# Performance work log

Hardware: AMD Instinct MI355X
Metric: run time of the kernel (lower is better)

The kernel has to match this reference:

```python
import jax, jax.numpy as jnp
import numpy as np

B, S, E, H = 2, 2048, 1024, 16
D = E // H  # head_dim = 64
SCALE = D ** -0.5
NEG = -1e9


def setup_inputs() -> dict:
    key = jax.random.key(0)
    ks = jax.random.split(key, 10)
    hidden_states = jax.random.normal(ks[0], (B, S, E), dtype=jnp.float32)
    # CLIP-style additive causal mask [B, 1, L, S]
    causal = jnp.where(jnp.tril(jnp.ones((S, S), dtype=bool)), 0.0, NEG).astype(jnp.float32)
    attn_mask = jnp.broadcast_to(causal, (B, 1, S, S))
    def lin(kw, kb):
        W = jax.random.normal(kw, (E, E), dtype=jnp.float32) * (E ** -0.5)
        b = jax.random.normal(kb, (E,), dtype=jnp.float32) * 0.02
        return W, b
    Wq, bq = lin(ks[1], ks[2])
    Wk, bk = lin(ks[3], ks[4])
    Wv, bv = lin(ks[5], ks[6])
    Wo, bo = lin(ks[7], ks[8])
    return {"hidden_states": hidden_states, "attn_mask": attn_mask,
            "Wq": Wq, "bq": bq, "Wk": Wk, "bk": bk,
            "Wv": Wv, "bv": bv, "Wo": Wo, "bo": bo}


def reference(hidden_states, attn_mask, Wq, bq, Wk, bk, Wv, bv, Wo, bo):
    b, L, e = hidden_states.shape
    # projections (nn.Linear: x @ W.T + b)
    def split_heads(x):
        return x.reshape(b, L, H, D).transpose(0, 2, 1, 3)  # [b,h,l,d]
    q = split_heads(hidden_states @ Wq.T + bq)
    k = split_heads(hidden_states @ Wk.T + bk)
    v = split_heads(hidden_states @ Wv.T + bv)
    # QK^T * scale + additive mask, softmax, AV (dropout_p = 0 in eval)
    scores = jnp.einsum('bhld,bhsd->bhls', q, k) * SCALE + attn_mask
    attn = jax.nn.softmax(scores, axis=-1)
    ctx = jnp.einsum('bhls,bhsd->bhld', attn, v)
    ctx = ctx.transpose(0, 2, 1, 3).reshape(b, L, e)
    return ctx @ Wo.T + bo
```

## Files before the change

### kernel.cpp

```cpp
#include <hip/hip_runtime.h>
#include <hip/hip_bf16.h>
#include <stdint.h>


typedef __hip_bfloat16 bf16;
typedef short bf16x8 __attribute__((ext_vector_type(8)));
typedef short bf16x4 __attribute__((ext_vector_type(4)));
typedef float f32x4 __attribute__((ext_vector_type(4)));

__device__ __forceinline__ f32x4 mfma16(bf16x8 a, bf16x8 b, f32x4 c) {
  return __builtin_amdgcn_mfma_f32_16x16x32_bf16(a, b, c, 0, 0, 0);
}

__device__ __forceinline__ f32x4 mfma_k16(bf16x4 a, bf16x4 b, f32x4 c) {
#if __has_builtin(__builtin_amdgcn_mfma_f32_16x16x16bf16_1k)
  return __builtin_amdgcn_mfma_f32_16x16x16bf16_1k(a, b, c, 0, 0, 0);
#else
  f32x4 d;
  asm volatile("v_mfma_f32_16x16x16_bf16 %0, %1, %2, %3\n\ts_nop 7\n\ts_nop 7"
               : "=v"(d)
               : "v"(a), "v"(b), "v"(c));
  return d;
#endif
}

__device__ __forceinline__ void async16(const void* g, void* l) {
  __builtin_amdgcn_global_load_lds((const __attribute__((address_space(1))) void*)g,
                                   (__attribute__((address_space(3))) void*)l, 16, 0, 0);
}

__global__ __launch_bounds__(256) void cvt_kernel(
    const float* __restrict__ hs, const float* __restrict__ Wq,
    const float* __restrict__ Wk, const float* __restrict__ Wv,
    const float* __restrict__ Wo, bf16* __restrict__ dst) {
  const size_t e = ((size_t)blockIdx.x * 256 + threadIdx.x) * 8;
  const float* src;
  size_t off;
  if (e < 4194304) {
    src = hs; off = e;
  } else {
    const size_t w = e - 4194304;
    const int wi = (int)(w >> 20);
    src = (wi == 0) ? Wq : (wi == 1) ? Wk : (wi == 2) ? Wv : Wo;
    off = w & 1048575;
  }
  const float4 a = *(const float4*)(src + off);
  const float4 b = *(const float4*)(src + off + 4);
  union { bf16 h[8]; uint4 u; } p;
  p.h[0] = __float2bfloat16(a.x); p.h[1] = __float2bfloat16(a.y);
  p.h[2] = __float2bfloat16(a.z); p.h[3] = __float2bfloat16(a.w);
  p.h[4] = __float2bfloat16(b.x); p.h[5] = __float2bfloat16(b.y);
  p.h[6] = __float2bfloat16(b.z); p.h[7] = __float2bfloat16(b.w);
  *(uint4*)(dst + e) = p.u;
}

__global__ __launch_bounds__(256, 3) void qkv_gemm(
    const bf16* __restrict__ X, const bf16* __restrict__ Wb,
    const float* __restrict__ bq, const float* __restrict__ bk,
    const float* __restrict__ bv, bf16* __restrict__ out) {
  constexpr int Kd = 1024;
  __shared__ bf16 sA[128 * 32];
  __shared__ bf16 sB[128 * 32];
  const int tid = threadIdx.x;
  const int wave = tid >> 6, lane = tid & 63;
  const int g = lane >> 4, ln = lane & 15;
  const int tM = blockIdx.y * 128, tN = blockIdx.x * 128;
  const int which = tN >> 10;
  const bf16* W = Wb + (size_t)which * 1048576;
  const float* bias = (which == 0) ? bq : (which == 1) ? bk : bv;
  const int tNl = tN & 1023;
  const float oscale = (which == 0) ? 0.18033688011112042f : 1.0f;
  const int wrow = (wave >> 1) * 64, wcol = (wave & 1) * 64;
  const f32x4 fz = {0.f, 0.f, 0.f, 0.f};

  f32x4 acc[4][4];
#pragma unroll
  for (int i = 0; i < 4; ++i)
#pragma unroll
    for (int j = 0; j < 4; ++j) acc[i][j] = fz;

  for (int k0 = 0; k0 < Kd; k0 += 32) {
    __syncthreads();
#pragma unroll
    for (int t = 0; t < 2; ++t) {
      const int c = tid + t * 256;
      const int row = c >> 2, col = (c & 3) << 3;
      async16(X + (size_t)(tM + row) * Kd + k0 + col, sA + c * 8);
      async16(W + (size_t)(tNl + row) * Kd + k0 + col, sB + c * 8);
    }
    __syncthreads();
    bf16x8 aF[4], bF[4];
#pragma unroll
    for (int i = 0; i < 4; ++i)
      aF[i] = *(const bf16x8*)(sA + (wrow + i * 16 + ln) * 32 + g * 8);
#pragma unroll
    for (int j = 0; j < 4; ++j)
      bF[j] = *(const bf16x8*)(sB + (wcol + j * 16 + ln) * 32 + g * 8);
#pragma unroll
    for (int i = 0; i < 4; ++i)
#pragma unroll
      for (int j = 0; j < 4; ++j) acc[i][j] = mfma16(aF[i], bF[j], acc[i][j]);
  }

  bf16* outw = out + (size_t)which * 4194304;
#pragma unroll
  for (int j = 0; j < 4; ++j) {
    const int nl = tNl + wcol + j * 16 + ln;
    const float bvf = bias[nl];
    const int h = nl >> 6, d = nl & 63;
#pragma unroll
    for (int i = 0; i < 4; ++i) {
#pragma unroll
      for (int r = 0; r < 4; ++r) {
        const int m = tM + wrow + i * 16 + g * 4 + r;
        const int b = m >> 11, s = m & 2047;
        const float v = (acc[i][j][r] + bvf) * oscale;
        outw[(((size_t)(b * 16 + h) * 2048 + s) << 6) + d] = __float2bfloat16(v);
      }
    }
  }
}

__global__ __launch_bounds__(256, 2) void out_gemm(
    const bf16* __restrict__ X, const bf16* __restrict__ W,
    const float* __restrict__ bias, float* __restrict__ out) {
  constexpr int Kd = 1024;
  __shared__ bf16 sA[128 * 32];
  __shared__ bf16 sB[64 * 32];
  const int tid = threadIdx.x;
  const int wave = tid >> 6, lane = tid & 63;
  const int g = lane >> 4, ln = lane & 15;
  const int tM = blockIdx.y * 128, tN = blockIdx.x * 64;
  const f32x4 fz = {0.f, 0.f, 0.f, 0.f};

  f32x4 acc[2][4];
#pragma unroll
  for (int i = 0; i < 2; ++i)
#pragma unroll
    for (int j = 0; j < 4; ++j) acc[i][j] = fz;

  for (int k0 = 0; k0 < Kd; k0 += 32) {
    __syncthreads();
#pragma unroll
    for (int t = 0; t < 2; ++t) {
      const int c = tid + t * 256;
      async16(X + (size_t)(tM + (c >> 2)) * Kd + k0 + ((c & 3) << 3), sA + c * 8);
    }
    async16(W + (size_t)(tN + (tid >> 2)) * Kd + k0 + ((tid & 3) << 3), sB + tid * 8);
    __syncthreads();
    bf16x8 aF[2], bF[4];
#pragma unroll
    for (int i = 0; i < 2; ++i)
      aF[i] = *(const bf16x8*)(sA + (wave * 32 + i * 16 + ln) * 32 + g * 8);
#pragma unroll
    for (int j = 0; j < 4; ++j)
      bF[j] = *(const bf16x8*)(sB + (j * 16 + ln) * 32 + g * 8);
#pragma unroll
    for (int i = 0; i < 2; ++i)
#pragma unroll
      for (int j = 0; j < 4; ++j) acc[i][j] = mfma16(aF[i], bF[j], acc[i][j]);
  }

#pragma unroll
  for (int j = 0; j < 4; ++j) {
    const int n = tN + j * 16 + ln;
    const float bvf = bias[n];
#pragma unroll
    for (int i = 0; i < 2; ++i)
#pragma unroll
      for (int r = 0; r < 4; ++r) {
        const int m = tM + wave * 32 + i * 16 + g * 4 + r;
        out[(size_t)m * 1024 + n] = acc[i][j][r] + bvf;
      }
  }
}

__global__ __launch_bounds__(256, 2) void attn_kernel(
    const bf16* __restrict__ Q, const bf16* __restrict__ K,
    const bf16* __restrict__ V, bf16* __restrict__ O) {
  constexpr int S = 2048, D = 64;
  __shared__ bf16 sK[64 * 72];
  __shared__ bf16 sVf[64 * 64];

  const int tid = threadIdx.x;
  const int w = tid >> 6, lane = tid & 63;
  const int g = lane >> 4, ln = lane & 15;
  const int pid = blockIdx.x;
  const int bh = blockIdx.y;
  const int b = bh >> 4, h = bh & 15;
  const f32x4 fz = {0.f, 0.f, 0.f, 0.f};

  const bf16* Qb = Q + (size_t)bh * S * D;
  const bf16* Kb = K + (size_t)bh * S * D;
  const bf16* Vb = V + (size_t)bh * S * D;

  const int kr0 = tid >> 3, kc0 = (tid & 7) << 3;
  int vsrc[2][4], vdst[2];
#pragma unroll
  for (int t = 0; t < 2; ++t) {
    const int c = tid + t * 256;
    const int u = c * 2;
    const int kbdb = u >> 6, vg = (u >> 4) & 3, l0 = u & 15;
    const int kb = kbdb >> 2, db = kbdb & 3;
#pragma unroll
    for (int i = 0; i < 4; ++i) vsrc[t][i] = (kb * 16 + vg * 4 + i) * 64 + db * 16 + l0;
    vdst[t] = c * 8;
  }

#pragma unroll
  for (int p = 0; p < 2; ++p) {
    const int qt = p ? (31 - pid) : pid;

    bf16x8 qf[2];
#pragma unroll
    for (int kc = 0; kc < 2; ++kc)
      qf[kc] = *(const bf16x8*)(Qb + (size_t)(qt * 64 + w * 16 + ln) * D + kc * 32 + g * 8);

    f32x4 oacc[4];
#pragma unroll
    for (int db = 0; db < 4; ++db) oacc[db] = fz;
    float lsum = 0.f;

    uint4 kreg0 = *(const uint4*)(Kb + (size_t)kr0 * D + kc0);
    uint4 kreg1 = *(const uint4*)(Kb + (size_t)(kr0 + 32) * D + kc0);
    uint32_t vreg[2][4];
#pragma unroll
    for (int t = 0; t < 2; ++t)
#pragma unroll
      for (int i = 0; i < 4; ++i) vreg[t][i] = *(const uint32_t*)(Vb + vsrc[t][i]);

    for (int kt = 0; kt <= qt; ++kt) {
      __syncthreads();
      *(uint4*)(sK + kr0 * 72 + kc0) = kreg0;
      *(uint4*)(sK + (kr0 + 32) * 72 + kc0) = kreg1;
#pragma unroll
      for (int t = 0; t < 2; ++t) {
        const uint32_t d0 = vreg[t][0], d1 = vreg[t][1], d2 = vreg[t][2], d3 = vreg[t][3];
        uint4 pk;
        pk.x = (d1 << 16) | (d0 & 0xffffu);
        pk.y = (d3 << 16) | (d2 & 0xffffu);
        pk.z = (d1 & 0xffff0000u) | (d0 >> 16);
        pk.w = (d3 & 0xffff0000u) | (d2 >> 16);
        *(uint4*)(sVf + vdst[t]) = pk;
      }
      __syncthreads();
      if (kt < qt) {
        const size_t nb = (size_t)(kt + 1) * 64;
        kreg0 = *(const uint4*)(Kb + (nb + kr0) * D + kc0);
        kreg1 = *(const uint4*)(Kb + (nb + kr0 + 32) * D + kc0);
#pragma unroll
        for (int t = 0; t < 2; ++t)
#pragma unroll
          for (int i = 0; i < 4; ++i)
            vreg[t][i] = *(const uint32_t*)(Vb + nb * D + vsrc[t][i]);
      }

      f32x4 sacc[4];
#pragma unroll
      for (int kb = 0; kb < 4; ++kb) sacc[kb] = fz;
#pragma unroll
      for (int kb = 0; kb < 4; ++kb) {
        const bf16x8 k0 = *(const bf16x8*)(sK + (kb * 16 + ln) * 72 + g * 8);
        const bf16x8 k1 = *(const bf16x8*)(sK + (kb * 16 + ln) * 72 + 32 + g * 8);
        sacc[kb] = mfma16(k0, qf[0], sacc[kb]);
        sacc[kb] = mfma16(k1, qf[1], sacc[kb]);
      }

      const bool diag = (kt == qt);
      const int qloc = w * 16 + ln;
      bf16x4 pa[4];
#pragma unroll
      for (int kb = 0; kb < 4; ++kb) {
        union { bf16 hh[4]; bf16x4 v; } pu;
#pragma unroll
        for (int r = 0; r < 4; ++r) {
          float pv = exp2f(sacc[kb][r]);
          if (diag && (kb * 16 + g * 4 + r > qloc)) pv = 0.f;
          lsum += pv;
          pu.hh[r] = __float2bfloat16(pv);
        }
        pa[kb] = pu.v;
      }

#pragma unroll
      for (int db = 0; db < 4; ++db) {
#pragma unroll
        for (int kb = 0; kb < 4; ++kb) {
          const bf16x4 vf =
              *(const bf16x4*)(sVf + ((kb * 4 + db) * 64 + g * 16 + ln) * 4);
          oacc[db] = mfma_k16(pa[kb], vf, oacc[db]);
        }
      }
    }

    lsum += __shfl_xor(lsum, 16);
    lsum += __shfl_xor(lsum, 32);
    float invl[4];
#pragma unroll
    for (int r = 0; r < 4; ++r) invl[r] = 1.0f / __shfl(lsum, g * 4 + r);

#pragma unroll
    for (int db = 0; db < 4; ++db)
#pragma unroll
      for (int r = 0; r < 4; ++r) {
        const int row = qt * 64 + w * 16 + g * 4 + r;
        const int col = db * 16 + ln;
        O[(((size_t)(b * 2048 + row) * 16 + h) << 6) + col] =
            __float2bfloat16(oacc[db][r] * invl[r]);
      }
  }
}

extern "C" void kernel_launch(void* const* d_in, const int* in_sizes, int n_in,
                              void* d_out, int out_size, void* d_ws, size_t ws_size,
                              hipStream_t stream) {
  const float* hs = (const float*)d_in[0];
  const float* Wq = (const float*)d_in[2];
  const float* bq = (const float*)d_in[3];
  const float* Wk = (const float*)d_in[4];
  const float* bk = (const float*)d_in[5];
  const float* Wv = (const float*)d_in[6];
  const float* bv = (const float*)d_in[7];
  const float* Wo = (const float*)d_in[8];
  const float* bo = (const float*)d_in[9];
  float* out = (float*)d_out;

  char* ws = (char*)d_ws;
  bf16* XW = (bf16*)ws;
  bf16* Xb = XW;
  bf16* W3b = XW + 4194304;
  bf16* Wob = XW + 7340032;
  bf16* Qw = (bf16*)(ws + (16u << 20));
  bf16* Kw = (bf16*)(ws + (24u << 20));
  bf16* Vw = (bf16*)(ws + (32u << 20));
  bf16* Cw = (bf16*)ws;

  const dim3 blk(256);
  cvt_kernel<<<4096, blk, 0, stream>>>(hs, Wq, Wk, Wv, Wo, XW);
  qkv_gemm<<<dim3(24, 32), blk, 0, stream>>>(Xb, W3b, bq, bk, bv, Qw);
  attn_kernel<<<dim3(16, 32), blk, 0, stream>>>(Qw, Kw, Vw, Cw);
  out_gemm<<<dim3(16, 32), blk, 0, stream>>>(Cw, Wob, bo, out);
}
```

Measured before the change: 212.2 us.

## Share K/V tile loads between paired query tiles in one pass

Each block previously ran two separate passes over the K/V tiles, one per paired query tile (pid and 31-pid), loading the shared prefix of K/V twice. The loops are merged into one pass over the longer tile's range, so each K/V tile is staged to LDS once and used by both query tiles while both are active. This halves the K/V global loads and syncs for the shared range and interleaves two independent MFMA chains, at the cost of roughly double the accumulator and probability registers, which may lower occupancy. The A-side exp2 is computed even when inactive, which adds some wasted VALU work.

```diff
diff --git a/kernel.cpp b/kernel.cpp
--- a/kernel.cpp
+++ b/kernel.cpp
@@ -194,6 +194,8 @@
   const bf16* Kb = K + (size_t)bh * S * D;
   const bf16* Vb = V + (size_t)bh * S * D;
 
+  const int qtA = pid, qtB = 31 - pid;
+
   const int kr0 = tid >> 3, kc0 = (tid & 7) << 3;
   int vsrc[2][4], vdst[2];
 #pragma unroll
@@ -207,98 +209,112 @@
     vdst[t] = c * 8;
   }
 
+  bf16x8 qfA[2], qfB[2];
+#pragma unroll
+  for (int kc = 0; kc < 2; ++kc) {
+    qfA[kc] = *(const bf16x8*)(Qb + (size_t)(qtA * 64 + w * 16 + ln) * D + kc * 32 + g * 8);
+    qfB[kc] = *(const bf16x8*)(Qb + (size_t)(qtB * 64 + w * 16 + ln) * D + kc * 32 + g * 8);
+  }
+
+  f32x4 oaccA[4], oaccB[4];
+#pragma unroll
+  for (int db = 0; db < 4; ++db) { oaccA[db] = fz; oaccB[db] = fz; }
+  float lsumA = 0.f, lsumB = 0.f;
+
+  uint4 kreg0 = *(const uint4*)(Kb + (size_t)kr0 * D + kc0);
+  uint4 kreg1 = *(const uint4*)(Kb + (size_t)(kr0 + 32) * D + kc0);
+  uint32_t vreg[2][4];
+#pragma unroll
+  for (int t = 0; t < 2; ++t)
+#pragma unroll
+    for (int i = 0; i < 4; ++i) vreg[t][i] = *(const uint32_t*)(Vb + vsrc[t][i]);
+
+  const int qloc = w * 16 + ln;
+
+  for (int kt = 0; kt <= qtB; ++kt) {
+    const bool dual = (kt <= qtA);
+    __syncthreads();
+    *(uint4*)(sK + kr0 * 72 + kc0) = kreg0;
+    *(uint4*)(sK + (kr0 + 32) * 72 + kc0) = kreg1;
+#pragma unroll
+    for (int t = 0; t < 2; ++t) {
+      const uint32_t d0 = vreg[t][0], d1 = vreg[t][1], d2 = vreg[t][2], d3 = vreg[t][3];
+      uint4 pk;
+      pk.x = (d1 << 16) | (d0 & 0xffffu);
+      pk.y = (d3 << 16) | (d2 & 0xffffu);
+      pk.z = (d1 & 0xffff0000u) | (d0 >> 16);
+      pk.w = (d3 & 0xffff0000u) | (d2 >> 16);
+      *(uint4*)(sVf + vdst[t]) = pk;
+    }
+    __syncthreads();
+    if (kt < qtB) {
+      const size_t nb = (size_t)(kt + 1) * 64;
+      kreg0 = *(const uint4*)(Kb + (nb + kr0) * D + kc0);
+      kreg1 = *(const uint4*)(Kb + (nb + kr0 + 32) * D + kc0);
+#pragma unroll
+      for (int t = 0; t < 2; ++t)
+#pragma unroll
+        for (int i = 0; i < 4; ++i)
+          vreg[t][i] = *(const uint32_t*)(Vb + nb * D + vsrc[t][i]);
+    }
+
+    f32x4 saccA[4], saccB[4];
+#pragma unroll
+    for (int kb = 0; kb < 4; ++kb) { saccA[kb] = fz; saccB[kb] = fz; }
+#pragma unroll
+    for (int kb = 0; kb < 4; ++kb) {
+      const bf16x8 k0 = *(const bf16x8*)(sK + (kb * 16 + ln) * 72 + g * 8);
+      const bf16x8 k1 = *(const bf16x8*)(sK + (kb * 16 + ln) * 72 + 32 + g * 8);
+      saccB[kb] = mfma16(k0, qfB[0], saccB[kb]);
+      saccB[kb] = mfma16(k1, qfB[1], saccB[kb]);
+      if (dual) {
+        saccA[kb] = mfma16(k0, qfA[0], saccA[kb]);
+        saccA[kb] = mfma16(k1, qfA[1], saccA[kb]);
+      }
+    }
+
+    const bool diagA = (kt == qtA), diagB = (kt == qtB);
+    bf16x4 paA[4], paB[4];
+#pragma unroll
+    for (int kb = 0; kb < 4; ++kb) {
+      union { bf16 hh[4]; bf16x4 v; } puA, puB;
+#pragma unroll
+      for (int r = 0; r < 4; ++r) {
+        const int srow = kb * 16 + g * 4 + r;
+        float pB = exp2f(saccB[kb][r]);
+        if (diagB && (srow > qloc)) pB = 0.f;
+        lsumB += pB;
+        puB.hh[r] = __float2bfloat16(pB);
+        float pA = exp2f(saccA[kb][r]);
+        if (diagA && (srow > qloc)) pA = 0.f;
+        if (dual) lsumA += pA;
+        puA.hh[r] = __float2bfloat16(pA);
+      }
+      paB[kb] = puB.v;
+      paA[kb] = puA.v;
+    }
+
+#pragma unroll
+    for (int db = 0; db < 4; ++db) {
+#pragma unroll
+      for (int kb = 0; kb < 4; ++kb) {
+        const bf16x4 vf = *(const bf16x4*)(sVf + ((kb * 4 + db) * 64 + g * 16 + ln) * 4);
+        oaccB[db] = mfma_k16(paB[kb], vf, oaccB[db]);
+        if (dual) oaccA[db] = mfma_k16(paA[kb], vf, oaccA[db]);
+      }
+    }
+  }
+
 #pragma unroll
   for (int p = 0; p < 2; ++p) {
-    const int qt = p ? (31 - pid) : pid;
-
-    bf16x8 qf[2];
-#pragma unroll
-    for (int kc = 0; kc < 2; ++kc)
-      qf[kc] = *(const bf16x8*)(Qb + (size_t)(qt * 64 + w * 16 + ln) * D + kc * 32 + g * 8);
-
-    f32x4 oacc[4];
-#pragma unroll
-    for (int db = 0; db < 4; ++db) oacc[db] = fz;
-    float lsum = 0.f;
-
-    uint4 kreg0 = *(const uint4*)(Kb + (size_t)kr0 * D + kc0);
-    uint4 kreg1 = *(const uint4*)(Kb + (size_t)(kr0 + 32) * D + kc0);
-    uint32_t vreg[2][4];
-#pragma unroll
-    for (int t = 0; t < 2; ++t)
-#pragma unroll
-      for (int i = 0; i < 4; ++i) vreg[t][i] = *(const uint32_t*)(Vb + vsrc[t][i]);
-
-    for (int kt = 0; kt <= qt; ++kt) {
-      __syncthreads();
-      *(uint4*)(sK + kr0 * 72 + kc0) = kreg0;
-      *(uint4*)(sK + (kr0 + 32) * 72 + kc0) = kreg1;
-#pragma unroll
-      for (int t = 0; t < 2; ++t) {
-        const uint32_t d0 = vreg[t][0], d1 = vreg[t][1], d2 = vreg[t][2], d3 = vreg[t][3];
-        uint4 pk;
-        pk.x = (d1 << 16) | (d0 & 0xffffu);
-        pk.y = (d3 << 16) | (d2 & 0xffffu);
-        pk.z = (d1 & 0xffff0000u) | (d0 >> 16);
-        pk.w = (d3 & 0xffff0000u) | (d2 >> 16);
-        *(uint4*)(sVf + vdst[t]) = pk;
-      }
-      __syncthreads();
-      if (kt < qt) {
-        const size_t nb = (size_t)(kt + 1) * 64;
-        kreg0 = *(const uint4*)(Kb + (nb + kr0) * D + kc0);
-        kreg1 = *(const uint4*)(Kb + (nb + kr0 + 32) * D + kc0);
-#pragma unroll
-        for (int t = 0; t < 2; ++t)
-#pragma unroll
-          for (int i = 0; i < 4; ++i)
-            vreg[t][i] = *(const uint32_t*)(Vb + nb * D + vsrc[t][i]);
-      }
-
-      f32x4 sacc[4];
-#pragma unroll
-      for (int kb = 0; kb < 4; ++kb) sacc[kb] = fz;
-#pragma unroll
-      for (int kb = 0; kb < 4; ++kb) {
-        const bf16x8 k0 = *(const bf16x8*)(sK + (kb * 16 + ln) * 72 + g * 8);
-        const bf16x8 k1 = *(const bf16x8*)(sK + (kb * 16 + ln) * 72 + 32 + g * 8);
-        sacc[kb] = mfma16(k0, qf[0], sacc[kb]);
-        sacc[kb] = mfma16(k1, qf[1], sacc[kb]);
-      }
-
-      const bool diag = (kt == qt);
-      const int qloc = w * 16 + ln;
-      bf16x4 pa[4];
-#pragma unroll
-      for (int kb = 0; kb < 4; ++kb) {
-        union { bf16 hh[4]; bf16x4 v; } pu;
-#pragma unroll
-        for (int r = 0; r < 4; ++r) {
-          float pv = exp2f(sacc[kb][r]);
-          if (diag && (kb * 16 + g * 4 + r > qloc)) pv = 0.f;
-          lsum += pv;
-          pu.hh[r] = __float2bfloat16(pv);
-        }
-        pa[kb] = pu.v;
-      }
-
-#pragma unroll
-      for (int db = 0; db < 4; ++db) {
-#pragma unroll
-        for (int kb = 0; kb < 4; ++kb) {
-          const bf16x4 vf =
-              *(const bf16x4*)(sVf + ((kb * 4 + db) * 64 + g * 16 + ln) * 4);
-          oacc[db] = mfma_k16(pa[kb], vf, oacc[db]);
-        }
-      }
-    }
-
+    const int qt = p ? qtB : qtA;
+    float lsum = p ? lsumB : lsumA;
+    const f32x4* oacc = p ? oaccB : oaccA;
     lsum += __shfl_xor(lsum, 16);
     lsum += __shfl_xor(lsum, 32);
     float invl[4];
 #pragma unroll
     for (int r = 0; r < 4; ++r) invl[r] = 1.0f / __shfl(lsum, g * 4 + r);
-
 #pragma unroll
     for (int db = 0; db < 4; ++db)
 #pragma unroll
```

Result: slower. 233.1 us (+9.9%).
